# Kernel optimization log

Hardware: AMD Instinct MI355X
Metric: run time of the kernel (lower is better)

## Reference

```python
import jax, jax.numpy as jnp
import numpy as np

B, N, K, DIM = 2, 20000, 16, 256


def _mlp(x, W, b):
    # torch nn.Linear: x @ W.T + b, then LeakyReLU(0.1)
    return jax.nn.leaky_relu(x @ W.T + b, negative_slope=0.1)


def _lfa(features, geom, idx, W, b):
    # features: [B, N, C]; geom: [B, N, K, 4]; idx: [B, N, K]
    t = _mlp(geom, W, b)                                  # [B, N, K, d_lfa]
    fn = jax.vmap(lambda f, i: f[i])(features, idx)       # gather neighbors: [B, N, K, C]
    # mean over K of concat == concat of means (faithful, avoids big concat)
    return jnp.concatenate([t.mean(axis=2), fn.mean(axis=2)], axis=-1)


def _linear_init(key, out_f, in_f):
    k1, k2 = jax.random.split(key)
    bound = 1.0 / np.sqrt(in_f)
    W = jax.random.uniform(k1, (out_f, in_f), jnp.float32, -bound, bound)
    b = jax.random.uniform(k2, (out_f,), jnp.float32, -bound, bound)
    return W, b


def setup_inputs() -> dict:
    key = jax.random.key(0)
    ks = jax.random.split(key, 8)
    W_init, b_init = _linear_init(ks[0], DIM // 4, DIM)
    W_l1, b_l1 = _linear_init(ks[1], DIM // 4, 4)
    W_l2, b_l2 = _linear_init(ks[2], DIM // 2, 4)
    W_fin, b_fin = _linear_init(ks[3], DIM, DIM)
    W_id, b_id = _linear_init(ks[4], DIM, DIM)
    return {
        "input_tensor": jax.random.normal(ks[5], (B, N, DIM), jnp.float32),
        "geometric_features": jax.random.normal(ks[6], (B, N, K, 4), jnp.float32),
        "neighbor_indices": jax.random.randint(ks[7], (B, N, K), 0, N, jnp.int64 if jax.config.jax_enable_x64 else jnp.int32),
        "W_init": W_init, "b_init": b_init,
        "W_l1": W_l1, "b_l1": b_l1,
        "W_l2": W_l2, "b_l2": b_l2,
        "W_fin": W_fin, "b_fin": b_fin,
        "W_id": W_id, "b_id": b_id,
    }


def reference(input_tensor, geometric_features, neighbor_indices,
              W_init, b_init, W_l1, b_l1, W_l2, b_l2,
              W_fin, b_fin, W_id, b_id):
    residual = input_tensor
    x = _mlp(input_tensor, W_init, b_init)                       # [B, N, dim/4]
    x = _lfa(x, geometric_features, neighbor_indices, W_l1, b_l1)  # [B, N, dim/2]
    x = _lfa(x, geometric_features, neighbor_indices, W_l2, b_l2)  # [B, N, dim]
    x = _mlp(x, W_fin, b_fin)
    return x + _mlp(residual, W_id, b_id)
```

## Files before the change

kernel.cpp:

```cpp
#include <hip/hip_runtime.h>
#include <hip/hip_bf16.h>

#define BN   40000
#define NPTS 20000
#define KNN  16
#define DIM  256

typedef __attribute__((ext_vector_type(8))) short bf16x8;
typedef __attribute__((ext_vector_type(4))) float f32x4;
typedef __attribute__((ext_vector_type(16))) float f32x16;

__device__ __forceinline__ float lrelu(float v) { return fmaxf(v, 0.1f * v); }
__device__ __forceinline__ float bs2f(short s) {
    union { unsigned u; float f; } c; c.u = ((unsigned)(unsigned short)s) << 16;
    return c.f;
}
__device__ __forceinline__ short f2bs(float f) {
    __hip_bfloat16 h = __float2bfloat16(f);
    return *reinterpret_cast<short*>(&h);
}
__device__ __forceinline__ bf16x8 ldf32_bf16x8(const float* p) {
    const float4 a = ((const float4*)p)[0];
    const float4 b = ((const float4*)p)[1];
    bf16x8 r;
    r[0]=f2bs(a.x); r[1]=f2bs(a.y); r[2]=f2bs(a.z); r[3]=f2bs(a.w);
    r[4]=f2bs(b.x); r[5]=f2bs(b.y); r[6]=f2bs(b.z); r[7]=f2bs(b.w);
    return r;
}

__device__ __forceinline__ void dma16(const void* g, void* l) {
    __builtin_amdgcn_global_load_lds(
        (const __attribute__((address_space(1))) unsigned int*)g,
        (__attribute__((address_space(3))) unsigned int*)l, 16, 0, 0);
}

__global__ void __launch_bounds__(256) prep_kernel(
    const int* __restrict__ idxw, int* __restrict__ flag,
    const float* __restrict__ Wf, const float* __restrict__ Wi,
    const float* __restrict__ Wn,
    short* __restrict__ Wt, short* __restrict__ Wnt)
{
    if (blockIdx.x == 0) {
        __shared__ int red[256];
        int t = threadIdx.x;
        int v = 0;
#pragma unroll
        for (int it = 0; it < 64; ++it)
            v |= idxw[2 * (t + it * 256) + 1];
        red[t] = v;
        __syncthreads();
        for (int s = 128; s > 0; s >>= 1) {
            if (t < s) red[t] |= red[t + s];
            __syncthreads();
        }
        if (t == 0) *flag = (red[0] != 0) ? 1 : 0;
        return;
    }
    int t = (blockIdx.x - 1) * 256 + threadIdx.x;
    if (t < 32768) {
        int mat = (t >> 14) & 1;
        int tt  = t & 16383;
        float4 v = mat ? ((const float4*)Wi)[tt] : ((const float4*)Wf)[tt];
        int n  = tt >> 6;
        int k  = (tt & 63) * 4;
        int kk = k >> 5, q = (k >> 3) & 3, j = k & 7;
        short4 o; o.x=f2bs(v.x); o.y=f2bs(v.y); o.z=f2bs(v.z); o.w=f2bs(v.w);
        *(short4*)(Wt + ((size_t)((kk*2 + mat)*4 + q))*2048 + n*8 + j) = o;
    } else {
        int tt = t - 32768;
        float4 v = ((const float4*)Wn)[tt];
        int n  = tt >> 6;
        int k  = (tt & 63) * 4;
        int kk = k >> 5, q = (k >> 3) & 3, j = k & 7;
        short4 o; o.x=f2bs(v.x); o.y=f2bs(v.y); o.z=f2bs(v.z); o.w=f2bs(v.w);
        *(short4*)(Wnt + ((size_t)((kk*4 + q)*64 + n))*8 + j) = o;
    }
}

__global__ void __launch_bounds__(256) stage2_kernel(
    const float* __restrict__ geom,
    const float* __restrict__ W1, const float* __restrict__ B1,
    const float* __restrict__ W2, const float* __restrict__ B2,
    const float* __restrict__ X,
    const short* __restrict__ Wnt,
    const float* __restrict__ b_init,
    __hip_bfloat16* __restrict__ x2,
    __hip_bfloat16* __restrict__ x3,
    __hip_bfloat16* __restrict__ x1)
{
    __shared__ short wbuf[16384];

    if (blockIdx.x >= 625) {
        int bid = blockIdx.x - 625;
        int t = threadIdx.x;
        int wave = t >> 6, lane = t & 63;
        int r = lane & 15, q = lane >> 4;
        {
            const char* W8 = (const char*)Wnt;
            char* L8 = (char*)wbuf;
#pragma unroll
            for (int rd = 0; rd < 8; ++rd) {
                int off = (wave * 8 + rd) * 1024 + lane * 16;
                dma16(W8 + off, L8 + off);
            }
        }
        int m0 = bid * 64 + wave * 16;
        const float* Xs = X + (size_t)(m0 + r) * DIM + q * 8;
        bf16x8 a[8];
#pragma unroll
        for (int kk = 0; kk < 8; ++kk) a[kk] = ldf32_bf16x8(Xs + kk * 32);
        __syncthreads();

        f32x4 acc[4];
#pragma unroll
        for (int nt = 0; nt < 4; ++nt) acc[nt] = (f32x4){0.f,0.f,0.f,0.f};
#pragma unroll
        for (int kk = 0; kk < 8; ++kk) {
#pragma unroll
            for (int nt = 0; nt < 4; ++nt) {
                bf16x8 b = *(const bf16x8*)&wbuf[((kk*4 + q)*64 + nt*16 + r) * 8];
                acc[nt] = __builtin_amdgcn_mfma_f32_16x16x32_bf16(a[kk], b, acc[nt], 0, 0, 0);
            }
        }
#pragma unroll
        for (int nt = 0; nt < 4; ++nt) {
            int col = nt * 16 + r;
            float bvx = b_init[col];
#pragma unroll
            for (int i = 0; i < 4; ++i) {
                float v = lrelu(acc[nt][i] + bvx);
                x1[(size_t)(m0 + q*4 + i) * 64 + col] = __float2bfloat16(v);
            }
        }
        return;
    }

    const int lane = threadIdx.x & 63;
    const int wv   = threadIdx.x >> 6;
    const int c31  = lane & 31;
    const int hi   = lane >> 5;
    const int wglob = blockIdx.x * 4 + wv;

    bf16x8 bfr[6]; float bv[6];
#pragma unroll
    for (int tt = 0; tt < 6; ++tt) {
        bfr[tt] = (bf16x8){0,0,0,0,0,0,0,0};
        const float* Wrow;
        if (tt < 2) { Wrow = W1 + (size_t)(tt*32 + c31) * 4;     bv[tt] = B1[tt*32 + c31]; }
        else        { Wrow = W2 + (size_t)((tt-2)*32 + c31) * 4; bv[tt] = B2[(tt-2)*32 + c31]; }
        if (hi == 0) {
            const float4 w4 = *(const float4*)Wrow;
            bfr[tt][0]=f2bs(w4.x); bfr[tt][1]=f2bs(w4.y);
            bfr[tt][2]=f2bs(w4.z); bfr[tt][3]=f2bs(w4.w);
        }
    }
    f32x16 ZR;
#pragma unroll
    for (int i = 0; i < 16; ++i) ZR[i] = 0.f;

    float4 g = (float4){0.f,0.f,0.f,0.f};
    if (hi == 0)
        g = *(const float4*)(geom +
            ((size_t)((wglob * 8) * 2 + (c31 >> 4)) * KNN + (c31 & 15)) * 4);

#pragma unroll
    for (int it = 0; it < 8; ++it) {
        const int p0 = (wglob * 8 + it) * 2;
        const float4 gc = g;
        if (it < 7 && hi == 0)
            g = *(const float4*)(geom +
                ((size_t)(p0 + 2 + (c31 >> 4)) * KNN + (c31 & 15)) * 4);

        bf16x8 a = (bf16x8){0,0,0,0,0,0,0,0};
        if (hi == 0) { a[0]=f2bs(gc.x); a[1]=f2bs(gc.y); a[2]=f2bs(gc.z); a[3]=f2bs(gc.w); }

        f32x16 acc[6];
#pragma unroll
        for (int tt = 0; tt < 6; ++tt)
            acc[tt] = __builtin_amdgcn_mfma_f32_32x32x16_bf16(a, bfr[tt], ZR, 0, 0, 0);

#pragma unroll
        for (int tt = 0; tt < 6; ++tt) {
            float sA = 0.f, sB = 0.f;
#pragma unroll
            for (int i = 0; i < 8; ++i)  sA += lrelu(acc[tt][i]     + bv[tt]);
#pragma unroll
            for (int i = 0; i < 8; ++i)  sB += lrelu(acc[tt][i + 8] + bv[tt]);
            sA += __shfl_xor(sA, 32, 64);
            sB += __shfl_xor(sB, 32, 64);
            const float s = (hi ? sB : sA) * (1.f / 16.f);
            const short v = f2bs(s);
            if (tt < 2) ((short*)x2)[(size_t)(p0 + hi) * 128 + tt*32 + c31] = v;
            else        ((short*)x3)[(size_t)(p0 + hi) * 256 + (tt-2)*32 + c31] = v;
        }
    }
}

__global__ void __launch_bounds__(256) gather1_kernel(
    const int* __restrict__ idxw, const int* __restrict__ flag,
    const __hip_bfloat16* __restrict__ x1,
    __hip_bfloat16* __restrict__ x2)
{
    int t = blockIdx.x * 256 + threadIdx.x;
    int p = t >> 3, j = t & 7;
    int lane = threadIdx.x & 63;
    int dual = (*flag == 0) ? 2 : 1;
    int base = (p >= NPTS) ? NPTS : 0;
    int i0 = idxw[((size_t)p * 16 + 2*j)     * dual];
    int i1 = idxw[((size_t)p * 16 + 2*j + 1) * dual];
    int g8 = lane & 56;
    float acc[8];
#pragma unroll
    for (int i = 0; i < 8; ++i) acc[i] = 0.f;
#pragma unroll
    for (int k = 0; k < 8; ++k) {
        int rA = base + __shfl(i0, g8 + k, 64);
        int rB = base + __shfl(i1, g8 + k, 64);
        bf16x8 vA = *(const bf16x8*)((const short*)x1 + (size_t)rA * 64 + j * 8);
        bf16x8 vB = *(const bf16x8*)((const short*)x1 + (size_t)rB * 64 + j * 8);
#pragma unroll
        for (int i = 0; i < 8; ++i) acc[i] += bs2f(vA[i]) + bs2f(vB[i]);
    }
    bf16x8 o;
#pragma unroll
    for (int i = 0; i < 8; ++i) o[i] = f2bs(acc[i] * (1.f/16.f));
    *(bf16x8*)((short*)x2 + (size_t)p * 128 + 64 + j * 8) = o;
}

__global__ void __launch_bounds__(256) gather2_kernel(
    const int* __restrict__ idxw, const int* __restrict__ flag,
    const __hip_bfloat16* __restrict__ x2,
    __hip_bfloat16* __restrict__ x3)
{
    int t = blockIdx.x * 256 + threadIdx.x;
    int p = t >> 4, j = t & 15;
    int lane = threadIdx.x & 63;
    int dual = (*flag == 0) ? 2 : 1;
    int base = (p >= NPTS) ? NPTS : 0;
    int myi = idxw[((size_t)p * 16 + j) * dual];
    int g16 = lane & 48;
    float acc[8];
#pragma unroll
    for (int i = 0; i < 8; ++i) acc[i] = 0.f;
#pragma unroll
    for (int k = 0; k < KNN; ++k) {
        int row = base + __shfl(myi, g16 + k, 64);
        bf16x8 v = *(const bf16x8*)((const short*)x2 + (size_t)row * 128 + j * 8);
#pragma unroll
        for (int i = 0; i < 8; ++i) acc[i] += bs2f(v[i]);
    }
    bf16x8 o;
#pragma unroll
    for (int i = 0; i < 8; ++i) o[i] = f2bs(acc[i] * (1.f/16.f));
    *(bf16x8*)((short*)x3 + (size_t)p * 256 + 128 + j * 8) = o;
}

__global__ void __launch_bounds__(512, 2) final_mfma(
    const __hip_bfloat16* __restrict__ X3,
    const float* __restrict__ RES,
    const short* __restrict__ Wt,
    const float* __restrict__ Bf,
    const float* __restrict__ Bi,
    float* __restrict__ OUT)
{
    __shared__ short lw[65536];
    const int t    = threadIdx.x;
    const int wave = t >> 6, lane = t & 63;
    const int r = lane & 15, q = lane >> 4;
    const int rg = wave >> 1, cg = wave & 1;
    const int ch = blockIdx.x & 1;
    const int p0 = (blockIdx.x >> 1) * 320;

    {
        const char* WtB = (const char*)Wt;
        char* L = (char*)lw;
#pragma unroll
        for (int i = 0; i < 16; ++i) {
            int c = wave * 8 + (i >> 1);
            int d = i & 1;
            int mat = c >> 5, kk = (c >> 2) & 7, qq = c & 3;
            int src_sh = ((kk * 2 + mat) * 4 + qq) * 2048 + ch * 1024;
            dma16(WtB + (size_t)src_sh * 2 + d * 1024 + lane * 16,
                  L + (c * 2 + d) * 1024 + lane * 16);
        }
    }
    const int cb = ch * 128 + cg * 64;
    float bfv[4], biv[4];
#pragma unroll
    for (int nt = 0; nt < 4; ++nt) {
        bfv[nt] = Bf[cb + nt * 16 + r];
        biv[nt] = Bi[cb + nt * 16 + r];
    }
    __syncthreads();

    const short* bpf = lw + q * 1024 + (cg * 64 + r) * 8;
    const short* bpi = bpf + 32768;

#pragma unroll
    for (int tt = 0; tt < 5; ++tt) {
        const int row = p0 + tt * 64 + rg * 16 + r;
        const short* x3r = (const short*)X3 + (size_t)row * DIM + q * 8;
        const float* rsr = RES + (size_t)row * DIM + q * 8;

        bf16x8 a1[8];
        float4 rw[16];
#pragma unroll
        for (int kk = 0; kk < 8; ++kk) {
            rw[2*kk]   = ((const float4*)rsr)[kk * 8];
            rw[2*kk+1] = ((const float4*)rsr)[kk * 8 + 1];
            a1[kk] = *(const bf16x8*)(x3r + kk * 32);
        }

        f32x4 acc1[4], acc2[4];
#pragma unroll
        for (int nt = 0; nt < 4; ++nt) {
            acc1[nt] = (f32x4){0.f,0.f,0.f,0.f};
            acc2[nt] = (f32x4){0.f,0.f,0.f,0.f};
        }
#pragma unroll
        for (int kk = 0; kk < 8; ++kk) {
            bf16x8 a2;
            {
                const float4 lo = rw[2*kk], hi = rw[2*kk+1];
                a2[0]=f2bs(lo.x); a2[1]=f2bs(lo.y); a2[2]=f2bs(lo.z); a2[3]=f2bs(lo.w);
                a2[4]=f2bs(hi.x); a2[5]=f2bs(hi.y); a2[6]=f2bs(hi.z); a2[7]=f2bs(hi.w);
            }
#pragma unroll
            for (int nt = 0; nt < 4; ++nt) {
                bf16x8 b1 = *(const bf16x8*)(bpf + kk * 4096 + nt * 128);
                bf16x8 b2 = *(const bf16x8*)(bpi + kk * 4096 + nt * 128);
                acc1[nt] = __builtin_amdgcn_mfma_f32_16x16x32_bf16(a1[kk], b1, acc1[nt], 0, 0, 0);
                acc2[nt] = __builtin_amdgcn_mfma_f32_16x16x32_bf16(a2,    b2, acc2[nt], 0, 0, 0);
            }
        }
#pragma unroll
        for (int nt = 0; nt < 4; ++nt) {
            const int col = cb + nt * 16 + r;
#pragma unroll
            for (int i = 0; i < 4; ++i) {
                float v = lrelu(acc1[nt][i] + bfv[nt]) + lrelu(acc2[nt][i] + biv[nt]);
                OUT[(size_t)(p0 + tt * 64 + rg * 16 + q * 4 + i) * DIM + col] = v;
            }
        }
    }
}

extern "C" void kernel_launch(void* const* d_in, const int* in_sizes, int n_in,
                              void* d_out, int out_size, void* d_ws, size_t ws_size,
                              hipStream_t stream)
{
    const float* input  = (const float*)d_in[0];
    const float* geom   = (const float*)d_in[1];
    const int*   idxw   = (const int*)d_in[2];
    const float* W_init = (const float*)d_in[3];
    const float* b_init = (const float*)d_in[4];
    const float* W_l1   = (const float*)d_in[5];
    const float* b_l1   = (const float*)d_in[6];
    const float* W_l2   = (const float*)d_in[7];
    const float* b_l2   = (const float*)d_in[8];
    const float* W_fin  = (const float*)d_in[9];
    const float* b_fin  = (const float*)d_in[10];
    const float* W_id   = (const float*)d_in[11];
    const float* b_id   = (const float*)d_in[12];
    float* out = (float*)d_out;

    char* ws = (char*)d_ws;
    int* flag = (int*)ws;
    short* Wt  = (short*)(ws + 16);
    short* Wnt = (short*)(ws + 16 + 262144);
    __hip_bfloat16* x2 = (__hip_bfloat16*)(ws + 16 + 5120000);
    __hip_bfloat16* x3 = (__hip_bfloat16*)(ws + 16 + 15360000);
    __hip_bfloat16* x1 = (__hip_bfloat16*)d_out;

    prep_kernel<<<145, 256, 0, stream>>>(idxw, flag, W_fin, W_id, W_init,
                                         Wt, Wnt);
    stage2_kernel<<<1250, 256, 0, stream>>>(geom, W_l1, b_l1, W_l2, b_l2,
                                            input, Wnt, b_init, x2, x3, x1);
    gather1_kernel<<<1250, 256, 0, stream>>>(idxw, flag, x1, x2);
    gather2_kernel<<<2500, 256, 0, stream>>>(idxw, flag, x2, x3);
    final_mfma<<<250, 512, 0, stream>>>(x3, input, Wt, b_fin, b_id, out);
}
```

Measured before the change: 195.8 us.

## Fold prep kernel into stage2 and convert W_init to bf16 in-block

Removes the separate prep kernel launch. Its W_fin/W_id transpose-conversion and the index-width flag reduction now run as extra blocks appended to stage2. The init-MLP blocks no longer read a pre-converted W_init copy; each block loads the fp32 W_init, converts it to bf16 and stores it into LDS itself. The X loads are also regrouped into batches before conversion. This saves one kernel launch and the global round trip for Wnt, at the cost of redundant per-block weight conversion and more global reads of fp32 weights.

```diff
diff --git a/kernel.cpp b/kernel.cpp
--- a/kernel.cpp
+++ b/kernel.cpp
@@ -19,14 +19,6 @@
     __hip_bfloat16 h = __float2bfloat16(f);
     return *reinterpret_cast<short*>(&h);
 }
-__device__ __forceinline__ bf16x8 ldf32_bf16x8(const float* p) {
-    const float4 a = ((const float4*)p)[0];
-    const float4 b = ((const float4*)p)[1];
-    bf16x8 r;
-    r[0]=f2bs(a.x); r[1]=f2bs(a.y); r[2]=f2bs(a.z); r[3]=f2bs(a.w);
-    r[4]=f2bs(b.x); r[5]=f2bs(b.y); r[6]=f2bs(b.z); r[7]=f2bs(b.w);
-    return r;
-}
 
 __device__ __forceinline__ void dma16(const void* g, void* l) {
     __builtin_amdgcn_global_load_lds(
@@ -34,30 +26,40 @@
         (__attribute__((address_space(3))) unsigned int*)l, 16, 0, 0);
 }
 
-__global__ void __launch_bounds__(256) prep_kernel(
-    const int* __restrict__ idxw, int* __restrict__ flag,
+__global__ void __launch_bounds__(256) stage2_kernel(
+    const float* __restrict__ geom,
+    const float* __restrict__ W1, const float* __restrict__ B1,
+    const float* __restrict__ W2, const float* __restrict__ B2,
+    const float* __restrict__ X,
+    const float* __restrict__ Wn,
+    const float* __restrict__ b_init,
+    const int* __restrict__ idxw,
     const float* __restrict__ Wf, const float* __restrict__ Wi,
-    const float* __restrict__ Wn,
-    short* __restrict__ Wt, short* __restrict__ Wnt)
-{
-    if (blockIdx.x == 0) {
-        __shared__ int red[256];
-        int t = threadIdx.x;
-        int v = 0;
-#pragma unroll
-        for (int it = 0; it < 64; ++it)
-            v |= idxw[2 * (t + it * 256) + 1];
-        red[t] = v;
-        __syncthreads();
-        for (int s = 128; s > 0; s >>= 1) {
-            if (t < s) red[t] |= red[t + s];
+    short* __restrict__ Wt, int* __restrict__ flag,
+    __hip_bfloat16* __restrict__ x2,
+    __hip_bfloat16* __restrict__ x3,
+    __hip_bfloat16* __restrict__ x1)
+{
+    __shared__ short wbuf[16384];
+
+    if (blockIdx.x >= 1250) {
+        if (blockIdx.x == 1378) {
+            __shared__ int red[256];
+            int t = threadIdx.x;
+            int v = 0;
+#pragma unroll
+            for (int it = 0; it < 64; ++it)
+                v |= idxw[2 * (t + it * 256) + 1];
+            red[t] = v;
             __syncthreads();
-        }
-        if (t == 0) *flag = (red[0] != 0) ? 1 : 0;
-        return;
-    }
-    int t = (blockIdx.x - 1) * 256 + threadIdx.x;
-    if (t < 32768) {
+            for (int s = 128; s > 0; s >>= 1) {
+                if (t < s) red[t] |= red[t + s];
+                __syncthreads();
+            }
+            if (t == 0) *flag = (red[0] != 0) ? 1 : 0;
+            return;
+        }
+        int t = (blockIdx.x - 1250) * 256 + threadIdx.x;
         int mat = (t >> 14) & 1;
         int tt  = t & 16383;
         float4 v = mat ? ((const float4*)Wi)[tt] : ((const float4*)Wf)[tt];
@@ -66,29 +68,8 @@
         int kk = k >> 5, q = (k >> 3) & 3, j = k & 7;
         short4 o; o.x=f2bs(v.x); o.y=f2bs(v.y); o.z=f2bs(v.z); o.w=f2bs(v.w);
         *(short4*)(Wt + ((size_t)((kk*2 + mat)*4 + q))*2048 + n*8 + j) = o;
-    } else {
-        int tt = t - 32768;
-        float4 v = ((const float4*)Wn)[tt];
-        int n  = tt >> 6;
-        int k  = (tt & 63) * 4;
-        int kk = k >> 5, q = (k >> 3) & 3, j = k & 7;
-        short4 o; o.x=f2bs(v.x); o.y=f2bs(v.y); o.z=f2bs(v.z); o.w=f2bs(v.w);
-        *(short4*)(Wnt + ((size_t)((kk*4 + q)*64 + n))*8 + j) = o;
-    }
-}
-
-__global__ void __launch_bounds__(256) stage2_kernel(
-    const float* __restrict__ geom,
-    const float* __restrict__ W1, const float* __restrict__ B1,
-    const float* __restrict__ W2, const float* __restrict__ B2,
-    const float* __restrict__ X,
-    const short* __restrict__ Wnt,
-    const float* __restrict__ b_init,
-    __hip_bfloat16* __restrict__ x2,
-    __hip_bfloat16* __restrict__ x3,
-    __hip_bfloat16* __restrict__ x1)
-{
-    __shared__ short wbuf[16384];
+        return;
+    }
 
     if (blockIdx.x >= 625) {
         int bid = blockIdx.x - 625;
@@ -96,19 +77,39 @@
         int wave = t >> 6, lane = t & 63;
         int r = lane & 15, q = lane >> 4;
         {
-            const char* W8 = (const char*)Wnt;
-            char* L8 = (char*)wbuf;
-#pragma unroll
-            for (int rd = 0; rd < 8; ++rd) {
-                int off = (wave * 8 + rd) * 1024 + lane * 16;
-                dma16(W8 + off, L8 + off);
+            const float4* Wn4 = (const float4*)Wn;
+#pragma unroll
+            for (int i = 0; i < 16; ++i) {
+                int o  = i * 256 + t;
+                int jh = o & 1;
+                int n  = (o >> 1) & 63;
+                int qq = (o >> 7) & 3;
+                int kk = o >> 9;
+                float4 v = Wn4[n * 64 + kk * 8 + qq * 2 + jh];
+                short4 s4; s4.x=f2bs(v.x); s4.y=f2bs(v.y); s4.z=f2bs(v.z); s4.w=f2bs(v.w);
+                *(short4*)&wbuf[o * 4] = s4;
             }
         }
         int m0 = bid * 64 + wave * 16;
-        const float* Xs = X + (size_t)(m0 + r) * DIM + q * 8;
+        const float4* X4 = (const float4*)(X + (size_t)(m0 + r) * DIM + q * 8);
         bf16x8 a[8];
 #pragma unroll
-        for (int kk = 0; kk < 8; ++kk) a[kk] = ldf32_bf16x8(Xs + kk * 32);
+        for (int g = 0; g < 2; ++g) {
+            float4 rwm[8];
+#pragma unroll
+            for (int kk = 0; kk < 4; ++kk) {
+                rwm[2*kk]   = X4[(g*4 + kk) * 8];
+                rwm[2*kk+1] = X4[(g*4 + kk) * 8 + 1];
+            }
+#pragma unroll
+            for (int kk = 0; kk < 4; ++kk) {
+                const float4 lo = rwm[2*kk], hi2 = rwm[2*kk+1];
+                bf16x8 av;
+                av[0]=f2bs(lo.x);  av[1]=f2bs(lo.y);  av[2]=f2bs(lo.z);  av[3]=f2bs(lo.w);
+                av[4]=f2bs(hi2.x); av[5]=f2bs(hi2.y); av[6]=f2bs(hi2.z); av[7]=f2bs(hi2.w);
+                a[g*4 + kk] = av;
+            }
+        }
         __syncthreads();
 
         f32x4 acc[4];
@@ -267,7 +268,7 @@
     const int t    = threadIdx.x;
     const int wave = t >> 6, lane = t & 63;
     const int r = lane & 15, q = lane >> 4;
-    const int rg = wave >> 1, cg = wave & 1;
+    const int rg = wave >> 1, cg2 = wave & 1;
     const int ch = blockIdx.x & 1;
     const int p0 = (blockIdx.x >> 1) * 320;
 
@@ -284,7 +285,7 @@
                   L + (c * 2 + d) * 1024 + lane * 16);
         }
     }
-    const int cb = ch * 128 + cg * 64;
+    const int cb = ch * 128 + cg2 * 64;
     float bfv[4], biv[4];
 #pragma unroll
     for (int nt = 0; nt < 4; ++nt) {
@@ -293,7 +294,7 @@
     }
     __syncthreads();
 
-    const short* bpf = lw + q * 1024 + (cg * 64 + r) * 8;
+    const short* bpf = lw + q * 1024 + (cg2 * 64 + r) * 8;
     const short* bpi = bpf + 32768;
 
 #pragma unroll
@@ -321,9 +322,9 @@
         for (int kk = 0; kk < 8; ++kk) {
             bf16x8 a2;
             {
-                const float4 lo = rw[2*kk], hi = rw[2*kk+1];
-                a2[0]=f2bs(lo.x); a2[1]=f2bs(lo.y); a2[2]=f2bs(lo.z); a2[3]=f2bs(lo.w);
-                a2[4]=f2bs(hi.x); a2[5]=f2bs(hi.y); a2[6]=f2bs(hi.z); a2[7]=f2bs(hi.w);
+                const float4 lo = rw[2*kk], hi2 = rw[2*kk+1];
+                a2[0]=f2bs(lo.x);  a2[1]=f2bs(lo.y);  a2[2]=f2bs(lo.z);  a2[3]=f2bs(lo.w);
+                a2[4]=f2bs(hi2.x); a2[5]=f2bs(hi2.y); a2[6]=f2bs(hi2.z); a2[7]=f2bs(hi2.w);
             }
 #pragma unroll
             for (int nt = 0; nt < 4; ++nt) {
@@ -367,15 +368,14 @@
     char* ws = (char*)d_ws;
     int* flag = (int*)ws;
     short* Wt  = (short*)(ws + 16);
-    short* Wnt = (short*)(ws + 16 + 262144);
     __hip_bfloat16* x2 = (__hip_bfloat16*)(ws + 16 + 5120000);
     __hip_bfloat16* x3 = (__hip_bfloat16*)(ws + 16 + 15360000);
     __hip_bfloat16* x1 = (__hip_bfloat16*)d_out;
 
-    prep_kernel<<<145, 256, 0, stream>>>(idxw, flag, W_fin, W_id, W_init,
-                                         Wt, Wnt);
-    stage2_kernel<<<1250, 256, 0, stream>>>(geom, W_l1, b_l1, W_l2, b_l2,
-                                            input, Wnt, b_init, x2, x3, x1);
+    stage2_kernel<<<1379, 256, 0, stream>>>(geom, W_l1, b_l1, W_l2, b_l2,
+                                            input, W_init, b_init,
+                                            idxw, W_fin, W_id, Wt, flag,
+                                            x2, x3, x1);
     gather1_kernel<<<1250, 256, 0, stream>>>(idxw, flag, x1, x2);
     gather2_kernel<<<2500, 256, 0, stream>>>(idxw, flag, x2, x3);
     final_mfma<<<250, 512, 0, stream>>>(x3, input, Wt, b_fin, b_id, out);
```

After: 198.3 us. Within noise of the previous version (+1.3%).
